# Kernel optimization log

Hardware: AMD Instinct MI355X
Metric: run time of the kernel (lower is better)

The kernel has to match this reference:

```python
import jax, jax.numpy as jnp
import numpy as np

B, S, E = 8, 2048, 1024

def setup_inputs() -> dict:
    key = jax.random.key(0)
    ks = jax.random.split(key, 7)
    scale = 1.0 / np.sqrt(E)
    return {
        "x": jax.random.normal(ks[0], (B, S, E), dtype=jnp.float32),
        "Wq": jax.random.normal(ks[1], (E, E), dtype=jnp.float32) * scale,
        "bq": jax.random.normal(ks[2], (E,), dtype=jnp.float32) * 0.01,
        "Wk": jax.random.normal(ks[3], (E, E), dtype=jnp.float32) * scale,
        "bk": jax.random.normal(ks[4], (E,), dtype=jnp.float32) * 0.01,
        "Wv": jax.random.normal(ks[5], (E, E), dtype=jnp.float32) * scale,
        "bv": jax.random.normal(ks[6], (E,), dtype=jnp.float32) * 0.01,
    }

def reference(x, Wq, bq, Wk, bk, Wv, bv):
    # torch Linear: y = x @ W^T + b
    q = jnp.einsum('bse,fe->bsf', x, Wq) + bq  # [B,S,E]
    k = jnp.einsum('bse,fe->bsf', x, Wk) + bk
    v = jnp.einsum('bse,fe->bsf', x, Wv) + bv
    # unscaled, unmasked single-head attention (faithful to source)
    scores = jnp.einsum('bqe,bke->bqk', q, k)  # [B,S,S]
    attn = jax.nn.softmax(scores, axis=-1)
    return jnp.einsum('bqk,bke->bqe', attn, v)  # [B,S,E]
```

## Files before the change

### kernel.cpp

```cpp
#include <hip/hip_runtime.h>
#include <math.h>

typedef _Float16 f16;
typedef _Float16 f16x8 __attribute__((ext_vector_type(8)));
typedef _Float16 f16x4 __attribute__((ext_vector_type(4)));
typedef float f32x4v __attribute__((ext_vector_type(4)));

#define Bb 8
#define Ss 2048
#define Ee 1024
#define BSr (Bb*Ss)
#define MB 1048576ull

__device__ __forceinline__ void gll16(const void* gp, void* lp) {
    __builtin_amdgcn_global_load_lds(
        (const __attribute__((address_space(1))) unsigned int*)gp,
        (__attribute__((address_space(3))) unsigned int*)lp,
        16, 0, 0);
}

#define MFMA16(a, b, c) __builtin_amdgcn_mfma_f32_16x16x32_f16((a), (b), (c), 0, 0, 0)
#define SBAR() asm volatile("s_barrier" ::: "memory")

__global__ __launch_bounds__(256)
void split_x(const float* __restrict__ x, f16* __restrict__ xh)
{
    const int i = (blockIdx.x * 256 + threadIdx.x) * 4;
    float4 v = *(const float4*)&x[i];
    f16x4 h4;
    h4[0] = (f16)v.x; h4[1] = (f16)v.y; h4[2] = (f16)v.z; h4[3] = (f16)v.w;
    *(f16x4*)&xh[i] = h4;
}

__global__ __launch_bounds__(256)
void split_wv(const float* __restrict__ Wv, f16* __restrict__ Wvh)
{
    const int i = (blockIdx.x * 256 + threadIdx.x) * 4;
    float4 v = *(const float4*)&Wv[i];
    f16x4 h4;
    h4[0] = (f16)v.x; h4[1] = (f16)v.y; h4[2] = (f16)v.z; h4[3] = (f16)v.w;
    *(f16x4*)&Wvh[i] = h4;
}

__global__ __launch_bounds__(256)
void transpose_split(const float* __restrict__ Wq, const float* __restrict__ Wk,
                     f16* __restrict__ WqTh, f16* __restrict__ WqTl,
                     f16* __restrict__ WkTh, f16* __restrict__ WkTl)
{
    __shared__ float ts[64][65];
    const int z = blockIdx.z;
    const float* W = z ? Wk : Wq;
    f16* Th = z ? WkTh : WqTh;
    f16* Tl = z ? WkTl : WqTl;
    const int e0 = blockIdx.x * 64, j0 = blockIdx.y * 64;
    const int t = threadIdx.x;
    {
        const int jj = t >> 2, c0 = (t & 3) * 16;
        #pragma unroll
        for (int m = 0; m < 4; ++m) {
            float4 v = *(const float4*)&W[(size_t)(j0 + jj) * Ee + e0 + c0 + m * 4];
            ts[jj][c0 + m*4 + 0] = v.x; ts[jj][c0 + m*4 + 1] = v.y;
            ts[jj][c0 + m*4 + 2] = v.z; ts[jj][c0 + m*4 + 3] = v.w;
        }
    }
    __syncthreads();
    {
        const int ee = t >> 2, jc0 = (t & 3) * 16;
        f16x8 h0, h1, l0, l1;
        #pragma unroll
        for (int m = 0; m < 16; ++m) {
            float val = ts[jc0 + m][ee];
            f16 hh = (f16)val; f16 ll = (f16)(val - (float)hh);
            if (m < 8) { h0[m] = hh; l0[m] = ll; }
            else       { h1[m-8] = hh; l1[m-8] = ll; }
        }
        size_t off = (size_t)(e0 + ee) * Ee + j0 + jc0;
        *(f16x8*)&Th[off]     = h0; *(f16x8*)&Th[off + 8] = h1;
        *(f16x8*)&Tl[off]     = l0; *(f16x8*)&Tl[off + 8] = l1;
    }
}

__global__ __launch_bounds__(256)
void compute_Mt(const f16* __restrict__ WkTh, const f16* __restrict__ WkTl,
                const f16* __restrict__ WqTh, const f16* __restrict__ WqTl,
                float* __restrict__ Mpart)
{
    __shared__ f16 Ah[128][32];
    __shared__ f16 Al[128][32];
    __shared__ f16 Bh[128][32];
    __shared__ f16 Bl[128][32];

    const int bn = blockIdx.x, bm = blockIdx.y, z = blockIdx.z;
    const int t = threadIdx.x;
    const int lane = t & 63;
    const int w = t >> 6;
    const int wr = w >> 1, wc = w & 1;
    const int lr = lane & 15;
    const int kq = (lane >> 4) << 3;
    const int rS = w * 32 + (lane >> 2);
    const int eS = (lane & 3) * 8;

    const f16* gAh = WkTh + ((size_t)(bm * 128 + rS)) * Ee + z * 256 + eS;
    const f16* gAl = WkTl + ((size_t)(bm * 128 + rS)) * Ee + z * 256 + eS;
    const f16* gBh = WqTh + ((size_t)(bn * 128 + rS)) * Ee + z * 256 + eS;
    const f16* gBl = WqTl + ((size_t)(bn * 128 + rS)) * Ee + z * 256 + eS;

    f32x4v acc[4][4];
    #pragma unroll
    for (int i = 0; i < 4; ++i)
        #pragma unroll
        for (int j = 0; j < 4; ++j) acc[i][j] = (f32x4v)0.f;

    for (int k0 = 0; k0 < 256; k0 += 32) {
        __syncthreads();
        #pragma unroll
        for (int c = 0; c < 2; ++c) {
            const size_t go = (size_t)c * 16 * Ee + k0;
            const int lo = w * 1024 + c * 512;
            gll16(gAh + go, &Ah[0][0] + lo);
            gll16(gAl + go, &Al[0][0] + lo);
            gll16(gBh + go, &Bh[0][0] + lo);
            gll16(gBl + go, &Bl[0][0] + lo);
        }
        __syncthreads();

        f16x8 fah[4], fal[4], fbh[4], fbl[4];
        #pragma unroll
        for (int i = 0; i < 4; ++i) {
            fah[i] = *(const f16x8*)&Ah[wr * 64 + i * 16 + lr][kq];
            fal[i] = *(const f16x8*)&Al[wr * 64 + i * 16 + lr][kq];
            fbh[i] = *(const f16x8*)&Bh[wc * 64 + i * 16 + lr][kq];
            fbl[i] = *(const f16x8*)&Bl[wc * 64 + i * 16 + lr][kq];
        }
        #pragma unroll
        for (int i = 0; i < 4; ++i)
            #pragma unroll
            for (int j = 0; j < 4; ++j) {
                acc[i][j] = MFMA16(fah[i], fbh[j], acc[i][j]);
                acc[i][j] = MFMA16(fah[i], fbl[j], acc[i][j]);
                acc[i][j] = MFMA16(fal[i], fbh[j], acc[i][j]);
            }
    }

    #pragma unroll
    for (int i = 0; i < 4; ++i) {
        #pragma unroll
        for (int j = 0; j < 4; ++j) {
            const int col = bn * 128 + wc * 64 + j * 16 + lr;
            #pragma unroll
            for (int r = 0; r < 4; ++r) {
                const int row = bm * 128 + wr * 64 + i * 16 + (lane >> 4) * 4 + r;
                Mpart[(size_t)z * MB + (size_t)row * Ee + col] = acc[i][j][r];
            }
        }
    }
}

__global__ __launch_bounds__(256)
void reduce_Mt(const float* __restrict__ Mpart, f16* __restrict__ Mth, f16* __restrict__ Mtl)
{
    const size_t i4 = ((size_t)blockIdx.x * 256 + threadIdx.x) * 4;
    float4 a = *(const float4*)&Mpart[i4];
    float4 b = *(const float4*)&Mpart[MB + i4];
    float4 c = *(const float4*)&Mpart[2 * MB + i4];
    float4 d = *(const float4*)&Mpart[3 * MB + i4];
    float s[4] = {a.x + b.x + c.x + d.x, a.y + b.y + c.y + d.y,
                  a.z + b.z + c.z + d.z, a.w + b.w + c.w + d.w};
    f16x4 h, l;
    #pragma unroll
    for (int m = 0; m < 4; ++m) { f16 hh = (f16)s[m]; h[m] = hh; l[m] = (f16)(s[m] - (float)hh); }
    *(f16x4*)&Mth[i4] = h;
    *(f16x4*)&Mtl[i4] = l;
}

__global__ __launch_bounds__(256)
void wker(const float* __restrict__ Wk, const float* __restrict__ bq,
          float* __restrict__ wpart)
{
    const int f = (blockIdx.x & 3) * 256 + threadIdx.x;
    const int p = blockIdx.x >> 2;
    float acc = 0.f;
    for (int j = p * 128; j < p * 128 + 128; ++j)
        acc += Wk[(size_t)j * Ee + f] * bq[j];
    wpart[p * Ee + f] = acc;
}

__global__ __launch_bounds__(256)
void vker(const f16* __restrict__ xh, const float* __restrict__ wpart,
          float* __restrict__ vbuf)
{
    __shared__ float wsum[1024];
    const int t = threadIdx.x;
    for (int ff = t; ff < 1024; ff += 256) {
        float s = 0.f;
        #pragma unroll
        for (int p = 0; p < 8; ++p) s += wpart[p * Ee + ff];
        wsum[ff] = s;
    }
    __syncthreads();
    const int lane = t & 63;
    const int row = blockIdx.x * 4 + (t >> 6);
    const f16* xr = xh + (size_t)row * Ee + lane * 16;
    f16x8 a = *(const f16x8*)&xr[0];
    f16x8 b = *(const f16x8*)&xr[8];
    float acc = 0.f;
    #pragma unroll
    for (int m = 0; m < 8; ++m) {
        acc += (float)a[m] * wsum[lane * 16 + m];
        acc += (float)b[m] * wsum[lane * 16 + 8 + m];
    }
    #pragma unroll
    for (int off = 1; off < 64; off <<= 1) acc += __shfl_xor(acc, off, 64);
    if (lane == 0) vbuf[row] = acc;
}

template<bool DUAL>
__device__ __forceinline__ void kloop32(
    const f16* __restrict__ Ag, const f16* __restrict__ Bhg,
    const f16* __restrict__ Blg, f16* __restrict__ lds,
    f32x4v acc[8][4], const int w, const int lane)
{
    constexpr int SETF = DUAL ? 24576 : 16384;
    const int wr = w >> 2, wc = w & 3;
    const int srcoff = (w * 16 + (lane & 15)) * Ee + (lane >> 4) * 8;
    const int lrd = lane * 8;
    const int NT = 32;

#define STAGE8(t, s) do {                                                   \
        const int k0_ = (t) * 32;                                           \
        const f16* gA_ = Ag + k0_ + srcoff;                                 \
        const f16* gB_ = Bhg + k0_ + srcoff;                                \
        f16* dA_ = lds + (s) * SETF + w * 512;                              \
        f16* dB_ = lds + (s) * SETF + 8192 + w * 512;                       \
        gll16(gA_,                       dA_);                              \
        gll16(gA_ + (size_t)8 * 16 * Ee, dA_ + 8 * 512);                    \
        gll16(gB_,                       dB_);                              \
        gll16(gB_ + (size_t)8 * 16 * Ee, dB_ + 8 * 512);                    \
        if (DUAL) {                                                         \
            const f16* gL_ = Blg + k0_ + srcoff;                            \
            f16* dL_ = lds + (s) * SETF + 16384 + w * 512;                  \
            gll16(gL_,                       dL_);                          \
            gll16(gL_ + (size_t)8 * 16 * Ee, dL_ + 8 * 512);                \
        }                                                                   \
    } while (0)

    STAGE8(0, 0);
    STAGE8(1, 1);
    if (DUAL) asm volatile("s_waitcnt vmcnt(6)" ::: "memory");
    else      asm volatile("s_waitcnt vmcnt(4)" ::: "memory");
    SBAR();

    for (int t = 0; t < NT; ++t) {
        const int s = t % 3;
        if (t + 2 < NT) STAGE8(t + 2, (t + 2) % 3);

        const f16* As = lds + s * SETF;
        const f16* Bh = As + 8192;
        const f16* Bl = As + 16384;
        f16x8 fa[8], fbh[4], fbl[4];
        #pragma unroll
        for (int i = 0; i < 8; ++i)
            fa[i] = *(const f16x8*)(As + (wr * 8 + i) * 512 + lrd);
        #pragma unroll
        for (int j = 0; j < 4; ++j)
            fbh[j] = *(const f16x8*)(Bh + (wc * 4 + j) * 512 + lrd);
        if (DUAL) {
            #pragma unroll
            for (int j = 0; j < 4; ++j)
                fbl[j] = *(const f16x8*)(Bl + (wc * 4 + j) * 512 + lrd);
        }
        #pragma unroll
        for (int j = 0; j < 4; ++j)
            #pragma unroll
            for (int i = 0; i < 8; ++i) {
                acc[i][j] = MFMA16(fa[i], fbh[j], acc[i][j]);
                if (DUAL)
                    acc[i][j] = MFMA16(fa[i], fbl[j], acc[i][j]);
            }

        if (t + 2 < NT) {
            if (DUAL) asm volatile("s_waitcnt vmcnt(6)" ::: "memory");
            else      asm volatile("s_waitcnt vmcnt(4)" ::: "memory");
        } else if (t + 1 < NT) {
            asm volatile("s_waitcnt vmcnt(0)" ::: "memory");
        }
        SBAR();
    }
#undef STAGE8
}

__global__ __launch_bounds__(512, 2)
void proj3(const f16* __restrict__ xh,
           const f16* __restrict__ Mth, const f16* __restrict__ Mtl,
           const f16* __restrict__ Wvh, const float* __restrict__ bv,
           f16* __restrict__ qp, f16* __restrict__ vT)
{
    __shared__ f16 lds[73728];

    const int lin = blockIdx.x;
    const int l = (lin & 7) * 64 + (lin >> 3);
    const int zc = l & 7;
    const int by = l >> 3;
    const int z = zc >> 2;
    const int col0 = (zc & 3) * 256;
    const int row0 = by * 256;

    const int t = threadIdx.x;
    const int lane = t & 63;
    const int w = t >> 6;
    const int wr = w >> 2, wc = w & 3;

    f32x4v acc[8][4];
    #pragma unroll
    for (int i = 0; i < 8; ++i)
        #pragma unroll
        for (int j = 0; j < 4; ++j) acc[i][j] = (f32x4v)0.f;

    const f16* Ax = xh + (size_t)row0 * Ee;
    if (z == 0) {
        kloop32<true>(Ax, Mth + (size_t)col0 * Ee, Mtl + (size_t)col0 * Ee,
                      lds, acc, w, lane);
        #pragma unroll
        for (int i = 0; i < 8; ++i) {
            #pragma unroll
            for (int j = 0; j < 4; ++j) {
                const int col = col0 + wc * 64 + j * 16 + (lane & 15);
                #pragma unroll
                for (int r = 0; r < 4; ++r) {
                    const int row = row0 + wr * 128 + i * 16 + (lane >> 4) * 4 + r;
                    qp[(size_t)row * Ee + col] = (f16)acc[i][j][r];
                }
            }
        }
    } else {
        kloop32<false>(Ax, Wvh + (size_t)col0 * Ee, Wvh + (size_t)col0 * Ee,
                       lds, acc, w, lane);
        #pragma unroll
        for (int i = 0; i < 8; ++i) {
            #pragma unroll
            for (int j = 0; j < 4; ++j) {
                const int e = col0 + wc * 64 + j * 16 + (lane & 15);
                const float b = bv[e];
                const int srow = row0 + wr * 128 + i * 16 + (lane >> 4) * 4;
                const int bb = srow >> 11;
                const int s = srow & 2047;
                f16x4 pk;
                #pragma unroll
                for (int r = 0; r < 4; ++r) pk[r] = (f16)(acc[i][j][r] + b);
                *(f16x4*)&vT[((size_t)bb * Ee + e) * Ss + s] = pk;
            }
        }
    }
}

__global__ __launch_bounds__(512, 2)
void score8(const f16* __restrict__ qp, const f16* __restrict__ xh,
            const float* __restrict__ vbuf, float* __restrict__ Sbuf, int batch0)
{
    __shared__ f16 lds[49152];

    const int lin = blockIdx.x;
    const int cpx = gridDim.x >> 3;
    const int l = (lin & 7) * cpx + (lin >> 3);
    const int bn = l & 7;
    const int bm = (l >> 3) & 7;
    const int zb = l >> 6;
    const int b = batch0 + zb;

    const int t = threadIdx.x;
    const int lane = t & 63;
    const int w = t >> 6;
    const int wr = w >> 2, wc = w & 3;

    const f16* Aq = qp + ((size_t)b * Ss + bm * 256) * Ee;
    const f16* Bk = xh + ((size_t)b * Ss + bn * 256) * Ee;

    f32x4v acc[8][4];
    #pragma unroll
    for (int i = 0; i < 8; ++i)
        #pragma unroll
        for (int j = 0; j < 4; ++j) acc[i][j] = (f32x4v)0.f;

    kloop32<false>(Aq, Bk, Bk, lds, acc, w, lane);

    #pragma unroll
    for (int i = 0; i < 8; ++i) {
        #pragma unroll
        for (int j = 0; j < 4; ++j) {
            const int col = bn * 256 + wc * 64 + j * 16 + (lane & 15);
            const float vv = vbuf[(size_t)b * Ss + col];
            #pragma unroll
            for (int r = 0; r < 4; ++r) {
                const int row = zb * Ss + bm * 256 + wr * 128 + i * 16 + (lane >> 4) * 4 + r;
                Sbuf[(size_t)row * 2048 + col] = acc[i][j][r] + vv;
            }
        }
    }
}

__global__ __launch_bounds__(256)
void softmax_rows(float* __restrict__ Sbuf)
{
    __shared__ float red[8];
    const int t = threadIdx.x;
    const int w = t >> 6;
    float* Srow = Sbuf + (size_t)blockIdx.x * 2048;

    float4 a = *(const float4*)&Srow[t * 8];
    float4 c = *(const float4*)&Srow[t * 8 + 4];
    float v[8] = {a.x, a.y, a.z, a.w, c.x, c.y, c.z, c.w};

    float m = v[0];
    #pragma unroll
    for (int i = 1; i < 8; ++i) m = fmaxf(m, v[i]);
    #pragma unroll
    for (int off = 1; off < 64; off <<= 1) m = fmaxf(m, __shfl_xor(m, off, 64));
    if ((t & 63) == 0) red[w] = m;
    __syncthreads();
    m = fmaxf(fmaxf(red[0], red[1]), fmaxf(red[2], red[3]));

    float e[8], s = 0.f;
    #pragma unroll
    for (int i = 0; i < 8; ++i) { e[i] = __expf(v[i] - m); s += e[i]; }
    #pragma unroll
    for (int off = 1; off < 64; off <<= 1) s += __shfl_xor(s, off, 64);
    if ((t & 63) == 0) red[4 + w] = s;
    __syncthreads();
    s = red[4] + red[5] + red[6] + red[7];

    const float inv = 1.0f / s;
    f16x8 pk;
    #pragma unroll
    for (int i = 0; i < 8; ++i) pk[i] = (f16)(e[i] * inv);
    *(f16x8*)(((f16*)Srow) + t * 8) = pk;
}

__global__ __launch_bounds__(256)
void pv_gemm(const float* __restrict__ Sbuf, const f16* __restrict__ vT,
             float* __restrict__ out, int batch0)
{
    __shared__ f16 Pt[128][32];
    __shared__ f16 Vt[128][32];

    const int zb = blockIdx.z;
    const int b = batch0 + zb;
    const int bm = blockIdx.y;
    const int bn = blockIdx.x;

    const int t = threadIdx.x;
    const int lane = t & 63;
    const int w = t >> 6;
    const int wr = w >> 1, wc = w & 1;
    const int lr = lane & 15;
    const int kq = (lane >> 4) << 3;

    const int rS = w * 32 + (lane >> 2);
    const int eS = (lane & 3) * 8;

    const f16* Pbase = (const f16*)Sbuf;
    const f16* gA = Pbase + ((size_t)(zb * Ss + bm * 128 + rS)) * 4096 + eS;
    const f16* gB = vT + ((size_t)b * Ee + bn * 128 + rS) * Ss + eS;

    f32x4v acc[4][4];
    #pragma unroll
    for (int i = 0; i < 4; ++i)
        #pragma unroll
        for (int j = 0; j < 4; ++j) acc[i][j] = (f32x4v)0.f;

    for (int k0 = 0; k0 < Ss; k0 += 32) {
        __syncthreads();
        #pragma unroll
        for (int c = 0; c < 2; ++c) {
            const int lo = w * 1024 + c * 512;
            gll16(gA + (size_t)c * 16 * 4096 + k0, &Pt[0][0] + lo);
            gll16(gB + (size_t)c * 16 * Ss + k0,   &Vt[0][0] + lo);
        }
        __syncthreads();

        f16x8 fa[4], fb[4];
        #pragma unroll
        for (int i = 0; i < 4; ++i) {
            fa[i] = *(const f16x8*)&Pt[wr * 64 + i * 16 + lr][kq];
            fb[i] = *(const f16x8*)&Vt[wc * 64 + i * 16 + lr][kq];
        }
        #pragma unroll
        for (int i = 0; i < 4; ++i)
            #pragma unroll
            for (int j = 0; j < 4; ++j)
                acc[i][j] = MFMA16(fa[i], fb[j], acc[i][j]);
    }

    #pragma unroll
    for (int i = 0; i < 4; ++i) {
        #pragma unroll
        for (int j = 0; j < 4; ++j) {
            const int col = bn * 128 + wc * 64 + j * 16 + lr;
            #pragma unroll
            for (int r = 0; r < 4; ++r) {
                const int row = bm * 128 + wr * 64 + i * 16 + (lane >> 4) * 4 + r;
                out[((size_t)b * Ss + row) * Ee + col] = acc[i][j][r];
            }
        }
    }
}

#define TQ 16
#define TK 256
#define EC 64
#define NCH (Ee/EC)
#define NT  (Ss/TK)

__global__ __launch_bounds__(256)
void qkv_gemm(const float* __restrict__ x,
              const float* __restrict__ Wq, const float* __restrict__ bq,
              const float* __restrict__ Wk, const float* __restrict__ bk,
              const float* __restrict__ Wv, const float* __restrict__ bv,
              float* __restrict__ oq, float* __restrict__ ok, float* __restrict__ ov)
{
    __shared__ float Xs[64][17];
    __shared__ float Ws[64][17];
    const int t = threadIdx.x;
    const int z = blockIdx.z;
    const float* __restrict__ W    = (z == 0) ? Wq : ((z == 1) ? Wk : Wv);
    const float* __restrict__ bias = (z == 0) ? bq : ((z == 1) ? bk : bv);
    float* __restrict__ out        = (z == 0) ? oq : ((z == 1) ? ok : ov);

    const int row0 = blockIdx.y << 6;
    const int col0 = blockIdx.x << 6;
    const int ti = t >> 4;
    const int tj = t & 15;
    const int lr = t >> 2;
    const int lc = (t & 3) << 2;

    float acc[4][4];
    #pragma unroll
    for (int i = 0; i < 4; ++i)
        #pragma unroll
        for (int j = 0; j < 4; ++j) acc[i][j] = 0.f;

    for (int e0 = 0; e0 < Ee; e0 += 16) {
        __syncthreads();
        {
            float4 xv = *(const float4*)&x[(row0 + lr)*Ee + e0 + lc];
            float4 wv = *(const float4*)&W[(col0 + lr)*Ee + e0 + lc];
            Xs[lr][lc]   = xv.x; Xs[lr][lc+1] = xv.y; Xs[lr][lc+2] = xv.z; Xs[lr][lc+3] = xv.w;
            Ws[lr][lc]   = wv.x; Ws[lr][lc+1] = wv.y; Ws[lr][lc+2] = wv.z; Ws[lr][lc+3] = wv.w;
        }
        __syncthreads();
        #pragma unroll
        for (int ee = 0; ee < 16; ++ee) {
            float xa[4], wb[4];
            #pragma unroll
            for (int i = 0; i < 4; ++i) xa[i] = Xs[(ti<<2)+i][ee];
            #pragma unroll
            for (int j = 0; j < 4; ++j) wb[j] = Ws[(tj<<2)+j][ee];
            #pragma unroll
            for (int i = 0; i < 4; ++i)
                #pragma unroll
                for (int j = 0; j < 4; ++j)
                    acc[i][j] = fmaf(xa[i], wb[j], acc[i][j]);
        }
    }

    const float4 b4 = *(const float4*)&bias[col0 + (tj<<2)];
    #pragma unroll
    for (int i = 0; i < 4; ++i) {
        float4 o;
        o.x = acc[i][0] + b4.x;
        o.y = acc[i][1] + b4.y;
        o.z = acc[i][2] + b4.z;
        o.w = acc[i][3] + b4.w;
        *(float4*)&out[(row0 + (ti<<2) + i)*Ee + col0 + (tj<<2)] = o;
    }
}

__global__ __launch_bounds__(256)
void flash_attn(const float* __restrict__ qsrc,
                const float* __restrict__ ksrc,
                const float* __restrict__ vsrc,
                float* __restrict__ out)
{
    __shared__ float qs[TQ][1028];
    __shared__ float kv[TK][68];
    __shared__ float ps[TQ][260];
    __shared__ float f_s[TQ];
    __shared__ float l_s[TQ];

    const int t = threadIdx.x;
    const int lane = t & 63;
    const int w = t >> 6;
    const int q0 = blockIdx.x * TQ;
    const int kb = (q0 / Ss) * Ss;

    {
        const int r = t >> 4;
        const int c0 = (t & 15) << 2;
        #pragma unroll
        for (int m = 0; m < 16; ++m) {
            float4 v4 = *(const float4*)&qsrc[(q0 + r)*Ee + c0 + (m << 6)];
            *(float4*)&qs[r][c0 + (m << 6)] = v4;
        }
    }

    float4 oacc[NCH];
    #pragma unroll
    for (int i = 0; i < NCH; ++i) oacc[i] = make_float4(0.f, 0.f, 0.f, 0.f);
    float m_reg[4], l_reg[4];
    #pragma unroll
    for (int i = 0; i < 4; ++i) { m_reg[i] = -INFINITY; l_reg[i] = 0.f; }

    const int ow = t >> 4;
    const int oc = (t & 15) << 2;

    for (int kt = 0; kt < NT; ++kt) {
        const int kr0 = kb + kt * TK;

        float sacc[4][4];
        #pragma unroll
        for (int i = 0; i < 4; ++i)
            #pragma unroll
            for (int j = 0; j < 4; ++j) sacc[i][j] = 0.f;

        for (int ec = 0; ec < NCH; ++ec) {
            __syncthreads();
            {
                const int rr = t >> 4;
                const int cc = (t & 15) << 2;
                #pragma unroll
                for (int m = 0; m < 16; ++m) {
                    float4 v4 = *(const float4*)&ksrc[(kr0 + rr + (m<<4))*Ee + ec*EC + cc];
                    *(float4*)&kv[rr + (m<<4)][cc] = v4;
                }
            }
            __syncthreads();
            #pragma unroll 4
            for (int ee = 0; ee < EC; ee += 4) {
                float4 q4[4];
                #pragma unroll
                for (int i = 0; i < 4; ++i)
                    q4[i] = *(const float4*)&qs[(w<<2)+i][ec*EC + ee];
                #pragma unroll
                for (int j = 0; j < 4; ++j) {
                    float4 k4 = *(const float4*)&kv[lane + (j<<6)][ee];
                    #pragma unroll
                    for (int i = 0; i < 4; ++i) {
                        sacc[i][j] = fmaf(q4[i].x, k4.x, sacc[i][j]);
                        sacc[i][j] = fmaf(q4[i].y, k4.y, sacc[i][j]);
                        sacc[i][j] = fmaf(q4[i].z, k4.z, sacc[i][j]);
                        sacc[i][j] = fmaf(q4[i].w, k4.w, sacc[i][j]);
                    }
                }
            }
        }

        float tmax[4];
        #pragma unroll
        for (int i = 0; i < 4; ++i)
            tmax[i] = fmaxf(fmaxf(sacc[i][0], sacc[i][1]), fmaxf(sacc[i][2], sacc[i][3]));
        #pragma unroll
        for (int off = 1; off < 64; off <<= 1) {
            #pragma unroll
            for (int i = 0; i < 4; ++i)
                tmax[i] = fmaxf(tmax[i], __shfl_xor(tmax[i], off, 64));
        }
        float rs[4], fi[4];
        #pragma unroll
        for (int i = 0; i < 4; ++i) {
            float mn = fmaxf(m_reg[i], tmax[i]);
            fi[i] = __expf(m_reg[i] - mn);
            m_reg[i] = mn;
            float r = 0.f;
            #pragma unroll
            for (int j = 0; j < 4; ++j) {
                float p = __expf(sacc[i][j] - mn);
                ps[(w<<2)+i][lane + (j<<6)] = p;
                r += p;
            }
            rs[i] = r;
        }
        #pragma unroll
        for (int off = 1; off < 64; off <<= 1) {
            #pragma unroll
            for (int i = 0; i < 4; ++i)
                rs[i] += __shfl_xor(rs[i], off, 64);
        }
        #pragma unroll
        for (int i = 0; i < 4; ++i)
            l_reg[i] = l_reg[i] * fi[i] + rs[i];
        if (lane == 0) {
            #pragma unroll
            for (int i = 0; i < 4; ++i) {
                f_s[(w<<2)+i] = fi[i];
                l_s[(w<<2)+i] = l_reg[i];
            }
        }
        __syncthreads();

        const float fown = f_s[ow];
        #pragma unroll
        for (int c4 = 0; c4 < NCH; ++c4) {
            oacc[c4].x *= fown; oacc[c4].y *= fown;
            oacc[c4].z *= fown; oacc[c4].w *= fown;
        }
        for (int pc = 0; pc < NCH; ++pc) {
            __syncthreads();
            {
                const int rr = t >> 4;
                const int cc = (t & 15) << 2;
                #pragma unroll
                for (int m = 0; m < 16; ++m) {
                    float4 v4 = *(const float4*)&vsrc[(kr0 + rr + (m<<4))*Ee + pc*EC + cc];
                    *(float4*)&kv[rr + (m<<4)][cc] = v4;
                }
            }
            __syncthreads();
            float4 acc = oacc[pc];
            #pragma unroll 4
            for (int tj0 = 0; tj0 < TK; tj0 += 4) {
                float4 p4 = *(const float4*)&ps[ow][tj0];
                float4 v0 = *(const float4*)&kv[tj0+0][oc];
                float4 v1 = *(const float4*)&kv[tj0+1][oc];
                float4 v2 = *(const float4*)&kv[tj0+2][oc];
                float4 v3 = *(const float4*)&kv[tj0+3][oc];
                acc.x = fmaf(p4.x, v0.x, acc.x); acc.y = fmaf(p4.x, v0.y, acc.y);
                acc.z = fmaf(p4.x, v0.z, acc.z); acc.w = fmaf(p4.x, v0.w, acc.w);
                acc.x = fmaf(p4.y, v1.x, acc.x); acc.y = fmaf(p4.y, v1.y, acc.y);
                acc.z = fmaf(p4.y, v1.z, acc.z); acc.w = fmaf(p4.y, v1.w, acc.w);
                acc.x = fmaf(p4.z, v2.x, acc.x); acc.y = fmaf(p4.z, v2.y, acc.y);
                acc.z = fmaf(p4.z, v2.z, acc.z); acc.w = fmaf(p4.z, v2.w, acc.w);
                acc.x = fmaf(p4.w, v3.x, acc.x); acc.y = fmaf(p4.w, v3.y, acc.y);
                acc.z = fmaf(p4.w, v3.z, acc.z); acc.w = fmaf(p4.w, v3.w, acc.w);
            }
            oacc[pc] = acc;
        }
    }

    __syncthreads();
    const float linv = 1.0f / l_s[ow];
    #pragma unroll
    for (int c4 = 0; c4 < NCH; ++c4) {
        float4 o = oacc[c4];
        o.x *= linv; o.y *= linv; o.z *= linv; o.w *= linv;
        *(float4*)&out[(q0 + ow)*Ee + oc + (c4 << 6)] = o;
    }
}

extern "C" void kernel_launch(void* const* d_in, const int* in_sizes, int n_in,
                              void* d_out, int out_size, void* d_ws, size_t ws_size,
                              hipStream_t stream)
{
    (void)in_sizes; (void)n_in; (void)out_size;
    const float* x  = (const float*)d_in[0];
    const float* Wq = (const float*)d_in[1];
    const float* bq = (const float*)d_in[2];
    const float* Wk = (const float*)d_in[3];
    const float* bk = (const float*)d_in[4];  (void)bk;
    const float* Wv = (const float*)d_in[5];
    const float* bv = (const float*)d_in[6];
    float* out = (float*)d_out;

    const size_t S4 = 64 * MB, S2 = 32 * MB;
    const size_t TAIL = 96 * MB + 16 * MB + MB;
    const size_t NEED4 = S4 + TAIL;
    const size_t NEED2 = S2 + TAIL;

    if (ws_size >= NEED2) {
        const int nb = (ws_size >= NEED4) ? 4 : 2;
        const size_t sb = (nb == 4) ? S4 : S2;
        char* base = (char*)d_ws;
        float* Sbuf = (float*)base;
        f16* xh   = (f16*)(base + sb);
        f16* qp   = (f16*)(base + sb + 32 * MB);
        f16* vT   = (f16*)(base + sb + 64 * MB);
        f16* Wvh  = (f16*)(base + sb + 96 * MB);
        f16* WqTh = (f16*)(base + sb + 98 * MB);
        f16* WqTl = (f16*)(base + sb + 100 * MB);
        f16* WkTh = (f16*)(base + sb + 102 * MB);
        f16* WkTl = (f16*)(base + sb + 104 * MB);
        f16* Mth  = (f16*)(base + sb + 106 * MB);
        f16* Mtl  = (f16*)(base + sb + 108 * MB);
        float* Mpart = (float*)(base + sb + 110 * MB);
        float* wpart = (float*)(base + sb + 126 * MB);
        float* vbuf  = (float*)(base + sb + 126 * MB + 65536);

        split_x<<<16384, 256, 0, stream>>>(x, xh);
        split_wv<<<1024, 256, 0, stream>>>(Wv, Wvh);
        transpose_split<<<dim3(16, 16, 2), 256, 0, stream>>>(Wq, Wk, WqTh, WqTl, WkTh, WkTl);
        compute_Mt<<<dim3(8, 8, 4), 256, 0, stream>>>(WkTh, WkTl, WqTh, WqTl, Mpart);
        reduce_Mt<<<1024, 256, 0, stream>>>(Mpart, Mth, Mtl);
        wker<<<32, 256, 0, stream>>>(Wk, bq, wpart);
        vker<<<4096, 256, 0, stream>>>(xh, wpart, vbuf);
        proj3<<<512, 512, 0, stream>>>(xh, Mth, Mtl, Wvh, bv, qp, vT);
        for (int c = 0; c < 8 / nb; ++c) {
            score8<<<64 * nb, 512, 0, stream>>>(qp, xh, vbuf, Sbuf, nb * c);
            softmax_rows<<<nb * 2048, 256, 0, stream>>>(Sbuf);
            pv_gemm<<<dim3(8, 16, nb), 256, 0, stream>>>(Sbuf, vT, out, nb * c);
        }
    } else {
        float* kbuf = (float*)d_ws;
        float* vbuf2 = kbuf + (size_t)BSr * Ee;
        dim3 g1(Ee / 64, BSr / 64, 3);
        qkv_gemm<<<g1, 256, 0, stream>>>(x, Wq, bq, Wk, bk, Wv, bv, out, kbuf, vbuf2);
        flash_attn<<<dim3(BSr / TQ), 256, 0, stream>>>(out, kbuf, vbuf2, out);
    }
}
```

Measured before the change: 420.8 us.

## Process all batches at once with a 256x256 MFMA PV kernel, merge split kernels

```diff
diff --git a/kernel.cpp b/kernel.cpp
--- a/kernel.cpp
+++ b/kernel.cpp
@@ -23,23 +23,17 @@
 #define SBAR() asm volatile("s_barrier" ::: "memory")
 
 __global__ __launch_bounds__(256)
-void split_x(const float* __restrict__ x, f16* __restrict__ xh)
-{
-    const int i = (blockIdx.x * 256 + threadIdx.x) * 4;
-    float4 v = *(const float4*)&x[i];
+void split_xw(const float* __restrict__ x, const float* __restrict__ Wv,
+              f16* __restrict__ xh, f16* __restrict__ Wvh)
+{
+    const int bid = blockIdx.x;
+    const float* src; f16* dst; int i;
+    if (bid < 16384) { src = x;  dst = xh;  i = (bid * 256 + threadIdx.x) * 4; }
+    else             { src = Wv; dst = Wvh; i = ((bid - 16384) * 256 + threadIdx.x) * 4; }
+    float4 v = *(const float4*)&src[i];
     f16x4 h4;
     h4[0] = (f16)v.x; h4[1] = (f16)v.y; h4[2] = (f16)v.z; h4[3] = (f16)v.w;
-    *(f16x4*)&xh[i] = h4;
-}
-
-__global__ __launch_bounds__(256)
-void split_wv(const float* __restrict__ Wv, f16* __restrict__ Wvh)
-{
-    const int i = (blockIdx.x * 256 + threadIdx.x) * 4;
-    float4 v = *(const float4*)&Wv[i];
-    f16x4 h4;
-    h4[0] = (f16)v.x; h4[1] = (f16)v.y; h4[2] = (f16)v.z; h4[3] = (f16)v.w;
-    *(f16x4*)&Wvh[i] = h4;
+    *(f16x4*)&dst[i] = h4;
 }
 
 __global__ __launch_bounds__(256)
@@ -216,31 +210,32 @@
 
 template<bool DUAL>
 __device__ __forceinline__ void kloop32(
-    const f16* __restrict__ Ag, const f16* __restrict__ Bhg,
-    const f16* __restrict__ Blg, f16* __restrict__ lds,
+    const f16* __restrict__ Ag, const int sA,
+    const f16* __restrict__ Bhg, const f16* __restrict__ Blg, const int sB,
+    const int NT, f16* __restrict__ lds,
     f32x4v acc[8][4], const int w, const int lane)
 {
     constexpr int SETF = DUAL ? 24576 : 16384;
     const int wr = w >> 2, wc = w & 3;
-    const int srcoff = (w * 16 + (lane & 15)) * Ee + (lane >> 4) * 8;
+    const int srcA = (w * 16 + (lane & 15)) * sA + (lane >> 4) * 8;
+    const int srcB = (w * 16 + (lane & 15)) * sB + (lane >> 4) * 8;
     const int lrd = lane * 8;
-    const int NT = 32;
 
 #define STAGE8(t, s) do {                                                   \
         const int k0_ = (t) * 32;                                           \
-        const f16* gA_ = Ag + k0_ + srcoff;                                 \
-        const f16* gB_ = Bhg + k0_ + srcoff;                                \
+        const f16* gA_ = Ag + k0_ + srcA;                                   \
+        const f16* gB_ = Bhg + k0_ + srcB;                                  \
         f16* dA_ = lds + (s) * SETF + w * 512;                              \
         f16* dB_ = lds + (s) * SETF + 8192 + w * 512;                       \
         gll16(gA_,                       dA_);                              \
-        gll16(gA_ + (size_t)8 * 16 * Ee, dA_ + 8 * 512);                    \
+        gll16(gA_ + (size_t)8 * 16 * sA, dA_ + 8 * 512);                    \
         gll16(gB_,                       dB_);                              \
-        gll16(gB_ + (size_t)8 * 16 * Ee, dB_ + 8 * 512);                    \
+        gll16(gB_ + (size_t)8 * 16 * sB, dB_ + 8 * 512);                    \
         if (DUAL) {                                                         \
-            const f16* gL_ = Blg + k0_ + srcoff;                            \
+            const f16* gL_ = Blg + k0_ + srcB;                              \
             f16* dL_ = lds + (s) * SETF + 16384 + w * 512;                  \
             gll16(gL_,                       dL_);                          \
-            gll16(gL_ + (size_t)8 * 16 * Ee, dL_ + 8 * 512);                \
+            gll16(gL_ + (size_t)8 * 16 * sB, dL_ + 8 * 512);                \
         }                                                                   \
     } while (0)
 
@@ -318,8 +313,8 @@
 
     const f16* Ax = xh + (size_t)row0 * Ee;
     if (z == 0) {
-        kloop32<true>(Ax, Mth + (size_t)col0 * Ee, Mtl + (size_t)col0 * Ee,
-                      lds, acc, w, lane);
+        kloop32<true>(Ax, Ee, Mth + (size_t)col0 * Ee, Mtl + (size_t)col0 * Ee, Ee,
+                      32, lds, acc, w, lane);
         #pragma unroll
         for (int i = 0; i < 8; ++i) {
             #pragma unroll
@@ -333,8 +328,8 @@
             }
         }
     } else {
-        kloop32<false>(Ax, Wvh + (size_t)col0 * Ee, Wvh + (size_t)col0 * Ee,
-                       lds, acc, w, lane);
+        kloop32<false>(Ax, Ee, Wvh + (size_t)col0 * Ee, Wvh + (size_t)col0 * Ee, Ee,
+                       32, lds, acc, w, lane);
         #pragma unroll
         for (int i = 0; i < 8; ++i) {
             #pragma unroll
@@ -381,7 +376,7 @@
         #pragma unroll
         for (int j = 0; j < 4; ++j) acc[i][j] = (f32x4v)0.f;
 
-    kloop32<false>(Aq, Bk, Bk, lds, acc, w, lane);
+    kloop32<false>(Aq, Ee, Bk, Bk, Ee, 32, lds, acc, w, lane);
 
     #pragma unroll
     for (int i = 0; i < 8; ++i) {
@@ -433,6 +428,48 @@
     #pragma unroll
     for (int i = 0; i < 8; ++i) pk[i] = (f16)(e[i] * inv);
     *(f16x8*)(((f16*)Srow) + t * 8) = pk;
+}
+
+__global__ __launch_bounds__(512, 2)
+void pv256(const float* __restrict__ Sbuf, const f16* __restrict__ vT,
+           float* __restrict__ out)
+{
+    __shared__ f16 lds[49152];
+
+    const int lin = blockIdx.x;
+    const int l = (lin & 7) * 32 + (lin >> 3);
+    const int bn = l & 3;
+    const int bm = (l >> 2) & 7;
+    const int b  = l >> 5;
+
+    const int t = threadIdx.x;
+    const int lane = t & 63;
+    const int w = t >> 6;
+    const int wr = w >> 2, wc = w & 3;
+
+    const f16* gA = (const f16*)Sbuf + ((size_t)(b * Ss + bm * 256)) * 4096;
+    const f16* gB = vT + ((size_t)b * Ee + bn * 256) * Ss;
+
+    f32x4v acc[8][4];
+    #pragma unroll
+    for (int i = 0; i < 8; ++i)
+        #pragma unroll
+        for (int j = 0; j < 4; ++j) acc[i][j] = (f32x4v)0.f;
+
+    kloop32<false>(gA, 4096, gB, gB, Ss, 64, lds, acc, w, lane);
+
+    #pragma unroll
+    for (int i = 0; i < 8; ++i) {
+        #pragma unroll
+        for (int j = 0; j < 4; ++j) {
+            const int col = bn * 256 + wc * 64 + j * 16 + (lane & 15);
+            #pragma unroll
+            for (int r = 0; r < 4; ++r) {
+                const int row = bm * 256 + wr * 128 + i * 16 + (lane >> 4) * 4 + r;
+                out[((size_t)b * Ss + row) * Ee + col] = acc[i][j][r];
+            }
+        }
+    }
 }
 
 __global__ __launch_bounds__(256)
@@ -759,14 +796,15 @@
     const float* bv = (const float*)d_in[6];
     float* out = (float*)d_out;
 
-    const size_t S4 = 64 * MB, S2 = 32 * MB;
+    const size_t S8 = 128 * MB, S4 = 64 * MB, S2 = 32 * MB;
     const size_t TAIL = 96 * MB + 16 * MB + MB;
+    const size_t NEED8 = S8 + TAIL;
     const size_t NEED4 = S4 + TAIL;
     const size_t NEED2 = S2 + TAIL;
 
     if (ws_size >= NEED2) {
-        const int nb = (ws_size >= NEED4) ? 4 : 2;
-        const size_t sb = (nb == 4) ? S4 : S2;
+        const int nb = (ws_size >= NEED8) ? 8 : ((ws_size >= NEED4) ? 4 : 2);
+        const size_t sb = (nb == 8) ? S8 : ((nb == 4) ? S4 : S2);
         char* base = (char*)d_ws;
         float* Sbuf = (float*)base;
         f16* xh   = (f16*)(base + sb);
@@ -783,18 +821,23 @@
         float* wpart = (float*)(base + sb + 126 * MB);
         float* vbuf  = (float*)(base + sb + 126 * MB + 65536);
 
-        split_x<<<16384, 256, 0, stream>>>(x, xh);
-        split_wv<<<1024, 256, 0, stream>>>(Wv, Wvh);
+        split_xw<<<17408, 256, 0, stream>>>(x, Wv, xh, Wvh);
         transpose_split<<<dim3(16, 16, 2), 256, 0, stream>>>(Wq, Wk, WqTh, WqTl, WkTh, WkTl);
         compute_Mt<<<dim3(8, 8, 4), 256, 0, stream>>>(WkTh, WkTl, WqTh, WqTl, Mpart);
         reduce_Mt<<<1024, 256, 0, stream>>>(Mpart, Mth, Mtl);
         wker<<<32, 256, 0, stream>>>(Wk, bq, wpart);
         vker<<<4096, 256, 0, stream>>>(xh, wpart, vbuf);
         proj3<<<512, 512, 0, stream>>>(xh, Mth, Mtl, Wvh, bv, qp, vT);
-        for (int c = 0; c < 8 / nb; ++c) {
-            score8<<<64 * nb, 512, 0, stream>>>(qp, xh, vbuf, Sbuf, nb * c);
-            softmax_rows<<<nb * 2048, 256, 0, stream>>>(Sbuf);
-            pv_gemm<<<dim3(8, 16, nb), 256, 0, stream>>>(Sbuf, vT, out, nb * c);
+        if (nb == 8) {
+            score8<<<512, 512, 0, stream>>>(qp, xh, vbuf, Sbuf, 0);
+            softmax_rows<<<16384, 256, 0, stream>>>(Sbuf);
+            pv256<<<256, 512, 0, stream>>>(Sbuf, vT, out);
+        } else {
+            for (int c = 0; c < 8 / nb; ++c) {
+                score8<<<64 * nb, 512, 0, stream>>>(qp, xh, vbuf, Sbuf, nb * c);
+                softmax_rows<<<nb * 2048, 256, 0, stream>>>(Sbuf);
+                pv_gemm<<<dim3(8, 16, nb), 256, 0, stream>>>(Sbuf, vT, out, nb * c);
+            }
         }
     } else {
         float* kbuf = (float*)d_ws;
```

New measurement: 362.9 us (median of 2 runs). -13.8%, faster.
